# Kernel optimization log

Hardware: AMD Instinct MI355X
Metric: run time of the kernel (lower is better)

The kernel has to match this reference:

```python
import jax, jax.numpy as jnp
import numpy as np

D_MODEL = 1024
NUM_HEADS = 16
D_K = D_MODEL // NUM_HEADS


def setup_inputs() -> dict:
    key = jax.random.key(0)
    ks = jax.random.split(key, 11)
    B, S = 2, 2048
    scale = 1.0 / np.sqrt(D_MODEL)
    return {
        "Q": jax.random.normal(ks[0], (B, S, D_MODEL), jnp.float32),
        "K": jax.random.normal(ks[1], (B, S, D_MODEL), jnp.float32),
        "V": jax.random.normal(ks[2], (B, S, D_MODEL), jnp.float32),
        "Wq": jax.random.normal(ks[3], (D_MODEL, D_MODEL), jnp.float32) * scale,
        "bq": jnp.zeros((D_MODEL,), jnp.float32),
        "Wk": jax.random.normal(ks[4], (D_MODEL, D_MODEL), jnp.float32) * scale,
        "bk": jnp.zeros((D_MODEL,), jnp.float32),
        "Wv": jax.random.normal(ks[5], (D_MODEL, D_MODEL), jnp.float32) * scale,
        "bv": jnp.zeros((D_MODEL,), jnp.float32),
        "Wo": jax.random.normal(ks[6], (D_MODEL, D_MODEL), jnp.float32) * scale,
        "bo": jnp.zeros((D_MODEL,), jnp.float32),
    }


def reference(Q, K, V, Wq, bq, Wk, bk, Wv, bv, Wo, bo):
    B, S, _ = Q.shape
    # linear projections (torch Linear: x @ W.T + b)
    q = Q @ Wq.T + bq
    k = K @ Wk.T + bk
    v = V @ Wv.T + bv
    # split heads: [B, S, H, d_k] -> [B, H, S, d_k]
    q = q.reshape(B, S, NUM_HEADS, D_K).transpose(0, 2, 1, 3)
    k = k.reshape(B, S, NUM_HEADS, D_K).transpose(0, 2, 1, 3)
    v = v.reshape(B, S, NUM_HEADS, D_K).transpose(0, 2, 1, 3)
    # scaled dot-product attention, full [B, H, S, S] scores as in original
    scores = jnp.einsum("bhqd,bhkd->bhqk", q, k) / jnp.sqrt(jnp.float32(D_K))
    probs = jax.nn.softmax(scores, axis=-1)
    attn = jnp.einsum("bhqk,bhkd->bhqd", probs, v)
    # merge heads and output projection
    attn = attn.transpose(0, 2, 1, 3).reshape(B, S, D_MODEL)
    return attn @ Wo.T + bo
```

## Files before the change

### kernel.cpp

```cpp
#include <hip/hip_runtime.h>
#include <cstdint>
#include <cstddef>

#define D_MODEL 1024
#define NHEADS 16
#define DK 64
#define BATCH 2
#define SEQ 2048
#define MROWS 4096

using f32x4 = __attribute__((ext_vector_type(4))) float;
using f32x16 = __attribute__((ext_vector_type(16))) float;
using u16x8 = __attribute__((ext_vector_type(8))) unsigned short;
using u32x4 = __attribute__((ext_vector_type(4))) unsigned int;
using bf16x8 = __attribute__((ext_vector_type(8))) __bf16;

static __device__ __forceinline__ f32x4 mfma16(u16x8 a, u16x8 b, f32x4 c) {
    return __builtin_amdgcn_mfma_f32_16x16x32_bf16(
        __builtin_bit_cast(bf16x8, a), __builtin_bit_cast(bf16x8, b), c, 0, 0, 0);
}
static __device__ __forceinline__ f32x16 mfma32(u16x8 a, u16x8 b, f32x16 c) {
    return __builtin_amdgcn_mfma_f32_32x32x16_bf16(
        __builtin_bit_cast(bf16x8, a), __builtin_bit_cast(bf16x8, b), c, 0, 0, 0);
}

static __device__ __forceinline__ unsigned short f2b(float f) {
    unsigned int u = __float_as_uint(f);
    u += 0x7fffu + ((u >> 16) & 1u);
    return (unsigned short)(u >> 16);
}
static __device__ __forceinline__ unsigned int cvt_pk(float lo, float hi) {
    unsigned int r;
    asm("v_cvt_pk_bf16_f32 %0, %1, %2" : "=v"(r) : "v"(lo), "v"(hi));
    return r;
}
static __device__ __forceinline__ void plswap(unsigned int& a, unsigned int& b) {
    asm("v_permlane32_swap_b32 %0, %1" : "+v"(a), "+v"(b));
}
static __device__ __forceinline__ float fexp2(float x) {
#if __has_builtin(__builtin_amdgcn_exp2f)
    return __builtin_amdgcn_exp2f(x);
#else
    float r;
    asm("v_exp_f32 %0, %1" : "=v"(r) : "v"(x));
    return r;
#endif
}
static __device__ __forceinline__ void gll16(const void* g, void* l) {
    __builtin_amdgcn_global_load_lds(
        (const __attribute__((address_space(1))) void*)g,
        (__attribute__((address_space(3))) void*)l, 16, 0, 0);
}
#define SBAR() __builtin_amdgcn_s_barrier()
#define SCHED0() __builtin_amdgcn_sched_barrier(0)

__global__ __launch_bounds__(256) void cvtw_kernel(const float* __restrict__ w0,
                                                   const float* __restrict__ w1,
                                                   const float* __restrict__ w2,
                                                   const float* __restrict__ w3,
                                                   unsigned short* __restrict__ out,
                                                   int n4, float scale0) {
    const float* srcs[4] = {w0, w1, w2, w3};
    const float* src = srcs[blockIdx.y];
    unsigned short* dst = out + (size_t)blockIdx.y * (size_t)n4 * 4;
    float scale = (blockIdx.y == 0) ? scale0 : 1.0f;
    int i = blockIdx.x * 256 + threadIdx.x;
    if (i < n4) {
        float4 v = reinterpret_cast<const float4*>(src)[i];
        ushort4 o;
        o.x = f2b(v.x * scale);
        o.y = f2b(v.y * scale);
        o.z = f2b(v.z * scale);
        o.w = f2b(v.w * scale);
        reinterpret_cast<ushort4*>(dst)[i] = o;
    }
}


__global__ __launch_bounds__(256, 3) void gemm_qkv_kernel(
    const float* __restrict__ A0, const float* __restrict__ A1, const float* __restrict__ A2,
    const unsigned short* __restrict__ W,
    unsigned short* __restrict__ qo, unsigned short* __restrict__ ko,
    unsigned short* __restrict__ vto,
    const float* __restrict__ b0, const float* __restrict__ b1, const float* __restrict__ b2,
    float qsc) {
    __shared__ __align__(16) char Asb[8192];
    __shared__ __align__(16) char Wb[2][8192];

    const int tid = threadIdx.x;
    const int lane = tid & 63;
    const int wid = tid >> 6;
    const int wr = wid >> 1, wc = wid & 1;
    const int g = (lane >> 4) & 3, l16 = lane & 15;

    const int logical = ((int)blockIdx.x & 7) * 96 + ((int)blockIdx.x >> 3);
    const int m = logical >> 8;
    const int rem = logical & 255;
    const int y = rem >> 3, xc = rem & 7;
    const int row0 = y * 128;
    const int wrow0 = m * 1024 + xc * 128;

    const float* Af = (m == 0) ? A0 : ((m == 1) ? A1 : A2);

    const int arow = tid >> 1;
    const int ahalf = tid & 1;
    const float* asrc = Af + (size_t)(row0 + arow) * 1024 + ahalf * 16;
    const int aline = tid >> 2;
    const int apar = (tid >> 1) & 1;
    const int al7 = aline & 7;
    const int aglo = ((apar * 4 + ahalf * 2) ^ al7) * 16;
    const int aghi = ((apar * 4 + ahalf * 2 + 1) ^ al7) * 16;

    const int sline = tid >> 3;
    const int sgl = (tid & 7) ^ (sline & 7);
    const int srow = sline * 2 + (sgl >> 2);
    const int skcol = (sgl & 3) * 8;

    float4 a0r, a1r, a2r, a3r;
    auto loadA = [&](int k0) {
        const float4* s = reinterpret_cast<const float4*>(asrc + k0);
        a0r = s[0];
        a1r = s[1];
        a2r = s[2];
        a3r = s[3];
    };
    auto writeA = [&]() {
        u32x4 glo = {cvt_pk(a0r.x, a0r.y), cvt_pk(a0r.z, a0r.w),
                     cvt_pk(a1r.x, a1r.y), cvt_pk(a1r.z, a1r.w)};
        u32x4 ghi = {cvt_pk(a2r.x, a2r.y), cvt_pk(a2r.z, a2r.w),
                     cvt_pk(a3r.x, a3r.y), cvt_pk(a3r.z, a3r.w)};
        *reinterpret_cast<u32x4*>(Asb + aline * 128 + aglo) = glo;
        *reinterpret_cast<u32x4*>(Asb + aline * 128 + aghi) = ghi;
    };
    auto stageW = [&](int k0, int buf) {
        const char* w0 = (const char*)W + (size_t)(wrow0 + srow) * 2048 + (size_t)(k0 + skcol) * 2;
        gll16(w0, Wb[buf] + wid * 1024);
        gll16(w0 + (size_t)64 * 2048, Wb[buf] + 4096 + wid * 1024);
    };

    const int rswz = ((((l16 & 1) << 2) + g) ^ ((l16 >> 1) & 7)) << 4;
    const int abase = (wr * 32 + (l16 >> 1)) * 128 + rswz;
    const int bbase = (wc * 32 + (l16 >> 1)) * 128 + rswz;

    f32x4 acc[4][4] = {};

    loadA(0);
    stageW(0, 0);
    asm volatile("s_waitcnt vmcnt(2)" ::: "memory");
    SCHED0();
    writeA();
    asm volatile("s_waitcnt lgkmcnt(0)" ::: "memory");
    SCHED0();

    for (int t = 0; t < 32; ++t) {
        if (t < 31) {
            loadA((t + 1) * 32);
            stageW((t + 1) * 32, (t & 1) ^ 1);
            asm volatile("s_waitcnt vmcnt(6)" ::: "memory");
        } else {
            asm volatile("s_waitcnt vmcnt(0)" ::: "memory");
        }
        SCHED0();
        SBAR();
        SCHED0();
        u16x8 af[4], bf[4];
#pragma unroll
        for (int mi = 0; mi < 4; ++mi)
            af[mi] = *reinterpret_cast<const u16x8*>(Asb + abase + mi * 1024);
#pragma unroll
        for (int ni = 0; ni < 4; ++ni)
            bf[ni] = *reinterpret_cast<const u16x8*>(Wb[t & 1] + bbase + ni * 1024);
        __builtin_amdgcn_s_setprio(1);
#pragma unroll
        for (int mi = 0; mi < 4; ++mi)
#pragma unroll
            for (int ni = 0; ni < 4; ++ni)
                acc[mi][ni] = mfma16(af[mi], bf[ni], acc[mi][ni]);
        __builtin_amdgcn_s_setprio(0);
        if (t < 31) {
            SBAR();
            SCHED0();
            asm volatile("s_waitcnt vmcnt(2)" ::: "memory");
            SCHED0();
            writeA();
            asm volatile("s_waitcnt lgkmcnt(0)" ::: "memory");
            SCHED0();
        }
    }

    const float* bias = (m == 0) ? b0 : ((m == 1) ? b1 : b2);
    const float bsc = (m == 0) ? qsc : 1.0f;
#pragma unroll
    for (int mi = 0; mi < 4; ++mi) {
#pragma unroll
        for (int ni = 0; ni < 4; ++ni) {
            int r = row0 + wr * 64 + mi * 16 + g * 4;
            int cl = xc * 128 + wc * 64 + ni * 16 + l16;
            float bv = bsc * bias[cl];
            if (m < 2) {
                unsigned short* outp = m ? ko : qo;
#pragma unroll
                for (int j = 0; j < 4; ++j)
                    outp[(size_t)(r + j) * 1024 + cl] = f2b(acc[mi][ni][j] + bv);
            } else {
                ushort4 o;
                o.x = f2b(acc[mi][ni][0] + bv);
                o.y = f2b(acc[mi][ni][1] + bv);
                o.z = f2b(acc[mi][ni][2] + bv);
                o.w = f2b(acc[mi][ni][3] + bv);
                *reinterpret_cast<ushort4*>(vto + (size_t)cl * MROWS + r) = o;
            }
        }
    }
}

__global__ __launch_bounds__(256, 4) void gemm_out_kernel(
    const unsigned short* __restrict__ Abf,
    const unsigned short* __restrict__ W,
    float* __restrict__ fo,
    const float* __restrict__ bias) {
    __shared__ __align__(16) char Ab[2][8192];
    __shared__ __align__(16) char Wb[2][4096];

    const int tid = threadIdx.x;
    const int lane = tid & 63;
    const int wid = tid >> 6;
    const int wr = wid >> 1, wc = wid & 1;
    const int g = (lane >> 4) & 3, l16 = lane & 15;

    const int logical = ((int)blockIdx.x & 7) * 64 + ((int)blockIdx.x >> 3);
    const int y = logical >> 4, xc = logical & 15;
    const int row0 = y * 128;
    const int wrow0 = xc * 64;

    const int sline = tid >> 3;
    const int sgl = (tid & 7) ^ (sline & 7);
    const int srow = sline * 2 + (sgl >> 2);
    const int skcol = (sgl & 3) * 8;

    auto stage = [&](int k0, int buf) {
        const char* a0 = (const char*)Abf + (size_t)(row0 + srow) * 2048 + (size_t)(k0 + skcol) * 2;
        gll16(a0, Ab[buf] + wid * 1024);
        gll16(a0 + (size_t)64 * 2048, Ab[buf] + 4096 + wid * 1024);
        const char* w0 = (const char*)W + (size_t)(wrow0 + srow) * 2048 + (size_t)(k0 + skcol) * 2;
        gll16(w0, Wb[buf] + wid * 1024);
    };

    const int rswz = ((((l16 & 1) << 2) + g) ^ ((l16 >> 1) & 7)) << 4;
    const int abase = (wr * 32 + (l16 >> 1)) * 128 + rswz;
    const int bbase = (wc * 16 + (l16 >> 1)) * 128 + rswz;

    f32x4 acc[4][2] = {};
    stage(0, 0);

    for (int t = 0; t < 32; ++t) {
        if (t < 31) stage((t + 1) * 32, (t & 1) ^ 1);
        if (t < 31) asm volatile("s_waitcnt vmcnt(3)" ::: "memory");
        else asm volatile("s_waitcnt vmcnt(0)" ::: "memory");
        SCHED0();
        SBAR();
        SCHED0();
        u16x8 af[4], bf[2];
#pragma unroll
        for (int mi = 0; mi < 4; ++mi)
            af[mi] = *reinterpret_cast<const u16x8*>(Ab[t & 1] + abase + mi * 1024);
#pragma unroll
        for (int ni = 0; ni < 2; ++ni)
            bf[ni] = *reinterpret_cast<const u16x8*>(Wb[t & 1] + bbase + ni * 1024);
        __builtin_amdgcn_s_setprio(1);
#pragma unroll
        for (int mi = 0; mi < 4; ++mi)
#pragma unroll
            for (int ni = 0; ni < 2; ++ni)
                acc[mi][ni] = mfma16(af[mi], bf[ni], acc[mi][ni]);
        __builtin_amdgcn_s_setprio(0);
        SBAR();
        SCHED0();
    }

#pragma unroll
    for (int mi = 0; mi < 4; ++mi) {
#pragma unroll
        for (int ni = 0; ni < 2; ++ni) {
            int r = row0 + wr * 64 + mi * 16 + g * 4;
            int cl = xc * 64 + wc * 32 + ni * 16 + l16;
            float bv = bias[cl];
#pragma unroll
            for (int j = 0; j < 4; ++j)
                fo[(size_t)(r + j) * 1024 + cl] = acc[mi][ni][j] + bv;
        }
    }
}

__global__ __launch_bounds__(512, 2) void attn_kernel(
    const unsigned short* __restrict__ qp,
    const unsigned short* __restrict__ kp,
    const unsigned short* __restrict__ vT,
    unsigned short* __restrict__ ao) {
    __shared__ __align__(16) char lds[65536];

    const int tid = threadIdx.x;
    const int lane = tid & 63;
    const int wid = tid >> 6;
    const int wq = wid & 3, wk = wid >> 2;
    const int l31 = lane & 31, hi = lane >> 5;

    const int logical = ((int)blockIdx.x & 7) * 64 + ((int)blockIdx.x >> 3);
    const int qt = logical & 15;
    const int bh = logical >> 4;
    const int b = bh >> 4, h = bh & 15;
    const int ch = h * DK;
    const int q0 = b * SEQ + qt * 128;

    const int srow = wid * 8 + (lane >> 3);
    const int g16 = (lane & 7) ^ (lane >> 3);
    const char* kbase = (const char*)kp + ((size_t)(b * SEQ + srow)) * 2048 + ch * 2 + g16 * 16;
    const char* vbase = (const char*)vT + ((size_t)(ch + srow)) * (MROWS * 2) + (size_t)b * SEQ * 2 + g16 * 16;

    const char* qr = (const char*)qp + (size_t)(q0 + wq * 32 + l31) * 2048 + ch * 2;
    u16x8 qf[4];
#pragma unroll
    for (int t = 0; t < 4; ++t)
        qf[t] = *reinterpret_cast<const u16x8*>(qr + t * 32 + hi * 16);

    auto stageKV = [&](int kt2, char* base) {
        gll16(kbase + (size_t)kt2 * (64 * 2048), base + wid * 1024);
        gll16(kbase + (size_t)(kt2 * 64 + 1024) * 2048, base + 8192 + wid * 1024);
        gll16(vbase + kt2 * 128, base + 16384 + wid * 1024);
        gll16(vbase + kt2 * 128 + 2048, base + 24576 + wid * 1024);
    };

    const int swz = (lane & 7) << 4;
    f32x16 acco[2] = {};
    float l0 = 0.f, l1 = 0.f, l2 = 0.f, l3 = 0.f;

    stageKV(0, lds);
    for (int kt = 0; kt < 16; ++kt) {
        if (kt < 15) stageKV(kt + 1, lds + (((kt + 1) & 1) << 15));
        if (kt < 15) asm volatile("s_waitcnt vmcnt(4)" ::: "memory");
        else asm volatile("s_waitcnt vmcnt(0)" ::: "memory");
        SCHED0();
        SBAR();
        SCHED0();
        const char* cb = lds + ((kt & 1) << 15);
        const char* Kb = cb + wk * 8192;
        const char* Vb = cb + 16384 + wk * 8192;

        unsigned int pf[4][4];
#pragma unroll
        for (int ts = 0; ts < 2; ++ts) {
            f32x16 s = {};
            __builtin_amdgcn_s_setprio(1);
#pragma unroll
            for (int t = 0; t < 4; ++t) {
                u16x8 kf = *reinterpret_cast<const u16x8*>(Kb + (ts * 32 + l31) * 128 + ((32 * t + 16 * hi) ^ swz));
                s = mfma32(kf, qf[t], s);
            }
            __builtin_amdgcn_s_setprio(0);
            float p[16];
#pragma unroll
            for (int r = 0; r < 16; r += 4) {
                p[r] = fexp2(s[r]);
                p[r + 1] = fexp2(s[r + 1]);
                p[r + 2] = fexp2(s[r + 2]);
                p[r + 3] = fexp2(s[r + 3]);
                l0 += p[r];
                l1 += p[r + 1];
                l2 += p[r + 2];
                l3 += p[r + 3];
            }
#pragma unroll
            for (int i = 0; i < 2; ++i) {
                unsigned int a = cvt_pk(p[2 * i], p[2 * i + 1]);
                unsigned int bb = cvt_pk(p[4 + 2 * i], p[5 + 2 * i]);
                plswap(a, bb);
                pf[2 * ts][i] = a;
                pf[2 * ts][i + 2] = bb;
                unsigned int a2 = cvt_pk(p[8 + 2 * i], p[9 + 2 * i]);
                unsigned int b2 = cvt_pk(p[12 + 2 * i], p[13 + 2 * i]);
                plswap(a2, b2);
                pf[2 * ts + 1][i] = a2;
                pf[2 * ts + 1][i + 2] = b2;
            }
        }
        __builtin_amdgcn_s_setprio(1);
#pragma unroll
        for (int t = 0; t < 4; ++t) {
            u32x4 wv = {pf[t][0], pf[t][1], pf[t][2], pf[t][3]};
            u16x8 pfr = __builtin_bit_cast(u16x8, wv);
#pragma unroll
            for (int dt = 0; dt < 2; ++dt) {
                u16x8 vf = *reinterpret_cast<const u16x8*>(Vb + (dt * 32 + l31) * 128 + ((32 * t + 16 * hi) ^ swz));
                acco[dt] = mfma32(vf, pfr, acco[dt]);
            }
        }
        __builtin_amdgcn_s_setprio(0);
        SBAR();
        SCHED0();
    }

    float L = (l0 + l1) + (l2 + l3);

    float Lh = L + __shfl_xor(L, 32);
    float* cmb = reinterpret_cast<float*>(lds);
    float* slot = cmb + (size_t)tid * 18;
    f32x16 outg = acco[1 ^ wk];
#pragma unroll
    for (int mm = 0; mm < 8; ++mm)
        *reinterpret_cast<float2*>(slot + 2 * mm) = float2{outg[2 * mm], outg[2 * mm + 1]};
    slot[16] = Lh;
    __syncthreads();
    const float* ps = cmb + (size_t)(tid ^ 256) * 18;
    f32x16 kept = acco[wk];
#pragma unroll
    for (int mm = 0; mm < 8; ++mm) {
        float2 t2 = *reinterpret_cast<const float2*>(ps + 2 * mm);
        kept[2 * mm] += t2.x;
        kept[2 * mm + 1] += t2.y;
    }
    float rl = 1.0f / (Lh + ps[16]);
    __syncthreads();

    char* ot = lds + wid * 2304;
    const int r7 = l31 & 7;
#pragma unroll
    for (int mm = 0; mm < 4; ++mm) {
        uint2 pko;
        pko.x = cvt_pk(kept[4 * mm] * rl, kept[4 * mm + 1] * rl);
        pko.y = cvt_pk(kept[4 * mm + 2] * rl, kept[4 * mm + 3] * rl);
        *reinterpret_cast<uint2*>(ot + l31 * 72 + (((2 * mm + hi) ^ r7) << 3)) = pko;
    }
    const int rr = lane >> 1, half = lane & 1;
    const int rb7 = rr & 7;
    uint2 t0 = *reinterpret_cast<const uint2*>(ot + rr * 72 + (((half * 4 + 0) ^ rb7) << 3));
    uint2 t1 = *reinterpret_cast<const uint2*>(ot + rr * 72 + (((half * 4 + 1) ^ rb7) << 3));
    uint2 t2 = *reinterpret_cast<const uint2*>(ot + rr * 72 + (((half * 4 + 2) ^ rb7) << 3));
    uint2 t3 = *reinterpret_cast<const uint2*>(ot + rr * 72 + (((half * 4 + 3) ^ rb7) << 3));
    unsigned short* dst = ao + (size_t)(q0 + wq * 32 + rr) * 1024 + ch + wk * 32 + half * 16;
    uint4 o0 = {t0.x, t0.y, t1.x, t1.y};
    uint4 o1 = {t2.x, t2.y, t3.x, t3.y};
    *reinterpret_cast<uint4*>(dst) = o0;
    *reinterpret_cast<uint4*>(dst + 8) = o1;
}

extern "C" void kernel_launch(void* const* d_in, const int* in_sizes, int n_in,
                              void* d_out, int out_size, void* d_ws, size_t ws_size,
                              hipStream_t stream) {
    const float* Q = (const float*)d_in[0];
    const float* K = (const float*)d_in[1];
    const float* V = (const float*)d_in[2];
    const float* Wq = (const float*)d_in[3];
    const float* bq = (const float*)d_in[4];
    const float* Wk = (const float*)d_in[5];
    const float* bk = (const float*)d_in[6];
    const float* Wv = (const float*)d_in[7];
    const float* bv = (const float*)d_in[8];
    const float* Wo = (const float*)d_in[9];
    const float* bo = (const float*)d_in[10];

    unsigned short* ws = (unsigned short*)d_ws;
    const size_t SZ = (size_t)MROWS * D_MODEL;
    const size_t WSZ = (size_t)D_MODEL * D_MODEL;
    unsigned short* bufW = ws;
    unsigned short* qp = bufW + 4 * WSZ;
    unsigned short* kp = qp + SZ;
    unsigned short* vT = kp + SZ;
    unsigned short* ao = vT + SZ;

    const float qscale = 0.125f * 1.44269504088896f;

    dim3 blk(256);
    dim3 gcw((unsigned)(WSZ / 4 / 256), 4);
    cvtw_kernel<<<gcw, blk, 0, stream>>>(Wq, Wk, Wv, Wo, bufW, (int)(WSZ / 4), qscale);

    gemm_qkv_kernel<<<dim3(768), blk, 0, stream>>>(Q, K, V, bufW, qp, kp, vT, bq, bk, bv, qscale);

    attn_kernel<<<dim3(512), dim3(512), 0, stream>>>(qp, kp, vT, ao);

    gemm_out_kernel<<<dim3(512), blk, 0, stream>>>(ao, bufW + 3 * WSZ, (float*)d_out, bo);
}
```

Baseline: 129.2 us.

## Deepen QKV GEMM A-prefetch and halve attention KV tile size

The QKV projection GEMM now prefetches two k-steps ahead, ping-ponging between two register sets for the fp32 A tile and issuing W stages earlier, to hide global load latency. The attention kernel shrinks its K/V tile from 64 to 32 keys per wave-half. This cuts LDS from 64KB to 36KB, which may allow more resident blocks per CU. In exchange it doubles the loop iterations and barriers and raises register pressure in the GEMM.

```diff
diff --git a/kernel.cpp b/kernel.cpp
--- a/kernel.cpp
+++ b/kernel.cpp
@@ -53,6 +53,8 @@
 }
 #define SBAR() __builtin_amdgcn_s_barrier()
 #define SCHED0() __builtin_amdgcn_sched_barrier(0)
+#define WAITV(n) asm volatile("s_waitcnt vmcnt(" #n ")" ::: "memory")
+#define WAITL0() asm volatile("s_waitcnt lgkmcnt(0)" ::: "memory")
 
 __global__ __launch_bounds__(256) void cvtw_kernel(const float* __restrict__ w0,
                                                    const float* __restrict__ w1,
@@ -77,6 +79,8 @@
 }
 
 
+struct AReg { float4 r0, r1, r2, r3; };
+
 __global__ __launch_bounds__(256, 3) void gemm_qkv_kernel(
     const float* __restrict__ A0, const float* __restrict__ A1, const float* __restrict__ A2,
     const unsigned short* __restrict__ W,
@@ -116,19 +120,19 @@
     const int srow = sline * 2 + (sgl >> 2);
     const int skcol = (sgl & 3) * 8;
 
-    float4 a0r, a1r, a2r, a3r;
-    auto loadA = [&](int k0) {
+    AReg rA, rB;
+    auto loadTo = [&](AReg& R, int k0) {
         const float4* s = reinterpret_cast<const float4*>(asrc + k0);
-        a0r = s[0];
-        a1r = s[1];
-        a2r = s[2];
-        a3r = s[3];
-    };
-    auto writeA = [&]() {
-        u32x4 glo = {cvt_pk(a0r.x, a0r.y), cvt_pk(a0r.z, a0r.w),
-                     cvt_pk(a1r.x, a1r.y), cvt_pk(a1r.z, a1r.w)};
-        u32x4 ghi = {cvt_pk(a2r.x, a2r.y), cvt_pk(a2r.z, a2r.w),
-                     cvt_pk(a3r.x, a3r.y), cvt_pk(a3r.z, a3r.w)};
+        R.r0 = s[0];
+        R.r1 = s[1];
+        R.r2 = s[2];
+        R.r3 = s[3];
+    };
+    auto writeFrom = [&](AReg& R) {
+        u32x4 glo = {cvt_pk(R.r0.x, R.r0.y), cvt_pk(R.r0.z, R.r0.w),
+                     cvt_pk(R.r1.x, R.r1.y), cvt_pk(R.r1.z, R.r1.w)};
+        u32x4 ghi = {cvt_pk(R.r2.x, R.r2.y), cvt_pk(R.r2.z, R.r2.w),
+                     cvt_pk(R.r3.x, R.r3.y), cvt_pk(R.r3.z, R.r3.w)};
         *reinterpret_cast<u32x4*>(Asb + aline * 128 + aglo) = glo;
         *reinterpret_cast<u32x4*>(Asb + aline * 128 + aghi) = ghi;
     };
@@ -144,22 +148,22 @@
 
     f32x4 acc[4][4] = {};
 
-    loadA(0);
+    loadTo(rA, 0);
+    loadTo(rB, 32);
     stageW(0, 0);
-    asm volatile("s_waitcnt vmcnt(2)" ::: "memory");
+    stageW(32, 1);
+    WAITV(8);
     SCHED0();
-    writeA();
-    asm volatile("s_waitcnt lgkmcnt(0)" ::: "memory");
+    writeFrom(rA);
+    WAITL0();
     SCHED0();
 
-    for (int t = 0; t < 32; ++t) {
-        if (t < 31) {
-            loadA((t + 1) * 32);
-            stageW((t + 1) * 32, (t & 1) ^ 1);
-            asm volatile("s_waitcnt vmcnt(6)" ::: "memory");
-        } else {
-            asm volatile("s_waitcnt vmcnt(0)" ::: "memory");
-        }
+    auto iter = [&](int t, AReg& ld, AReg& wr_) {
+        if (t < 30) loadTo(ld, (t + 2) * 32);
+        if (t == 0) WAITV(6);
+        else if (t < 30) WAITV(10);
+        else if (t == 30) WAITV(6);
+        else WAITV(0);
         SCHED0();
         SBAR();
         SCHED0();
@@ -180,12 +184,19 @@
         if (t < 31) {
             SBAR();
             SCHED0();
-            asm volatile("s_waitcnt vmcnt(2)" ::: "memory");
+            if (t < 30) stageW((t + 2) * 32, t & 1);
+            if (t < 30) WAITV(8);
+            else WAITV(2);
             SCHED0();
-            writeA();
-            asm volatile("s_waitcnt lgkmcnt(0)" ::: "memory");
+            writeFrom(wr_);
+            WAITL0();
             SCHED0();
         }
+    };
+#pragma unroll 1
+    for (int tt = 0; tt < 16; ++tt) {
+        iter(2 * tt, rA, rB);
+        iter(2 * tt + 1, rB, rA);
     }
 
     const float* bias = (m == 0) ? b0 : ((m == 1) ? b1 : b2);
@@ -255,8 +266,8 @@
 
     for (int t = 0; t < 32; ++t) {
         if (t < 31) stage((t + 1) * 32, (t & 1) ^ 1);
-        if (t < 31) asm volatile("s_waitcnt vmcnt(3)" ::: "memory");
-        else asm volatile("s_waitcnt vmcnt(0)" ::: "memory");
+        if (t < 31) WAITV(3);
+        else WAITV(0);
         SCHED0();
         SBAR();
         SCHED0();
@@ -297,7 +308,7 @@
     const unsigned short* __restrict__ kp,
     const unsigned short* __restrict__ vT,
     unsigned short* __restrict__ ao) {
-    __shared__ __align__(16) char lds[65536];
+    __shared__ __align__(16) char lds[36864];
 
     const int tid = threadIdx.x;
     const int lane = tid & 63;
@@ -312,10 +323,15 @@
     const int ch = h * DK;
     const int q0 = b * SEQ + qt * 128;
 
-    const int srow = wid * 8 + (lane >> 3);
-    const int g16 = (lane & 7) ^ (lane >> 3);
-    const char* kbase = (const char*)kp + ((size_t)(b * SEQ + srow)) * 2048 + ch * 2 + g16 * 16;
-    const char* vbase = (const char*)vT + ((size_t)(ch + srow)) * (MROWS * 2) + (size_t)b * SEQ * 2 + g16 * 16;
+    const int kline = tid >> 3;
+    const int krow = kline & 31;
+    const int kgl = (tid & 7) ^ (krow & 7);
+    const char* ksrc = (const char*)kp +
+        ((size_t)(b * SEQ + (kline >> 5) * 1024 + krow)) * 2048 + ch * 2 + kgl * 16;
+    const int vd = tid >> 3;
+    const int vgl = (tid & 7) ^ (vd & 7);
+    const char* vsrc = (const char*)vT + ((size_t)(ch + vd)) * (MROWS * 2) +
+        ((size_t)(b * SEQ + (vgl >> 2) * 1024 + (vgl & 3) * 8)) * 2;
 
     const char* qr = (const char*)qp + (size_t)(q0 + wq * 32 + l31) * 2048 + ch * 2;
     u16x8 qf[4];
@@ -324,73 +340,74 @@
         qf[t] = *reinterpret_cast<const u16x8*>(qr + t * 32 + hi * 16);
 
     auto stageKV = [&](int kt2, char* base) {
-        gll16(kbase + (size_t)kt2 * (64 * 2048), base + wid * 1024);
-        gll16(kbase + (size_t)(kt2 * 64 + 1024) * 2048, base + 8192 + wid * 1024);
-        gll16(vbase + kt2 * 128, base + 16384 + wid * 1024);
-        gll16(vbase + kt2 * 128 + 2048, base + 24576 + wid * 1024);
-    };
-
-    const int swz = (lane & 7) << 4;
+        gll16(ksrc + (size_t)kt2 * 65536, base + wid * 1024);
+        gll16(vsrc + kt2 * 64, base + 8192 + wid * 1024);
+    };
+
+    const int sw7 = (l31 & 7);
     f32x16 acco[2] = {};
     float l0 = 0.f, l1 = 0.f, l2 = 0.f, l3 = 0.f;
 
     stageKV(0, lds);
-    for (int kt = 0; kt < 16; ++kt) {
-        if (kt < 15) stageKV(kt + 1, lds + (((kt + 1) & 1) << 15));
-        if (kt < 15) asm volatile("s_waitcnt vmcnt(4)" ::: "memory");
-        else asm volatile("s_waitcnt vmcnt(0)" ::: "memory");
+    for (int kt = 0; kt < 32; ++kt) {
+        if (kt < 31) {
+            stageKV(kt + 1, lds + (((kt + 1) & 1) << 14));
+            WAITV(2);
+        } else {
+            WAITV(0);
+        }
         SCHED0();
         SBAR();
         SCHED0();
-        const char* cb = lds + ((kt & 1) << 15);
-        const char* Kb = cb + wk * 8192;
-        const char* Vb = cb + 16384 + wk * 8192;
-
-        unsigned int pf[4][4];
-#pragma unroll
-        for (int ts = 0; ts < 2; ++ts) {
-            f32x16 s = {};
-            __builtin_amdgcn_s_setprio(1);
-#pragma unroll
-            for (int t = 0; t < 4; ++t) {
-                u16x8 kf = *reinterpret_cast<const u16x8*>(Kb + (ts * 32 + l31) * 128 + ((32 * t + 16 * hi) ^ swz));
-                s = mfma32(kf, qf[t], s);
-            }
-            __builtin_amdgcn_s_setprio(0);
-            float p[16];
-#pragma unroll
-            for (int r = 0; r < 16; r += 4) {
-                p[r] = fexp2(s[r]);
-                p[r + 1] = fexp2(s[r + 1]);
-                p[r + 2] = fexp2(s[r + 2]);
-                p[r + 3] = fexp2(s[r + 3]);
-                l0 += p[r];
-                l1 += p[r + 1];
-                l2 += p[r + 2];
-                l3 += p[r + 3];
-            }
-#pragma unroll
-            for (int i = 0; i < 2; ++i) {
-                unsigned int a = cvt_pk(p[2 * i], p[2 * i + 1]);
-                unsigned int bb = cvt_pk(p[4 + 2 * i], p[5 + 2 * i]);
-                plswap(a, bb);
-                pf[2 * ts][i] = a;
-                pf[2 * ts][i + 2] = bb;
-                unsigned int a2 = cvt_pk(p[8 + 2 * i], p[9 + 2 * i]);
-                unsigned int b2 = cvt_pk(p[12 + 2 * i], p[13 + 2 * i]);
-                plswap(a2, b2);
-                pf[2 * ts + 1][i] = a2;
-                pf[2 * ts + 1][i + 2] = b2;
-            }
-        }
+        const char* cb = lds + ((kt & 1) << 14);
+
+        f32x16 s = {};
         __builtin_amdgcn_s_setprio(1);
 #pragma unroll
         for (int t = 0; t < 4; ++t) {
-            u32x4 wv = {pf[t][0], pf[t][1], pf[t][2], pf[t][3]};
+            u16x8 kf = *reinterpret_cast<const u16x8*>(
+                cb + wk * 4096 + l31 * 128 + (((2 * t + hi) ^ sw7) << 4));
+            s = mfma32(kf, qf[t], s);
+        }
+        __builtin_amdgcn_s_setprio(0);
+
+        float p[16];
+#pragma unroll
+        for (int r = 0; r < 16; r += 4) {
+            p[r] = fexp2(s[r]);
+            p[r + 1] = fexp2(s[r + 1]);
+            p[r + 2] = fexp2(s[r + 2]);
+            p[r + 3] = fexp2(s[r + 3]);
+            l0 += p[r];
+            l1 += p[r + 1];
+            l2 += p[r + 2];
+            l3 += p[r + 3];
+        }
+        unsigned int pf0[4], pf1[4];
+#pragma unroll
+        for (int i = 0; i < 2; ++i) {
+            unsigned int a = cvt_pk(p[2 * i], p[2 * i + 1]);
+            unsigned int bb = cvt_pk(p[4 + 2 * i], p[5 + 2 * i]);
+            plswap(a, bb);
+            pf0[i] = a;
+            pf0[i + 2] = bb;
+            unsigned int a2 = cvt_pk(p[8 + 2 * i], p[9 + 2 * i]);
+            unsigned int b2 = cvt_pk(p[12 + 2 * i], p[13 + 2 * i]);
+            plswap(a2, b2);
+            pf1[i] = a2;
+            pf1[i + 2] = b2;
+        }
+
+        __builtin_amdgcn_s_setprio(1);
+#pragma unroll
+        for (int t = 0; t < 2; ++t) {
+            u32x4 wv = t ? u32x4{pf1[0], pf1[1], pf1[2], pf1[3]}
+                         : u32x4{pf0[0], pf0[1], pf0[2], pf0[3]};
             u16x8 pfr = __builtin_bit_cast(u16x8, wv);
 #pragma unroll
             for (int dt = 0; dt < 2; ++dt) {
-                u16x8 vf = *reinterpret_cast<const u16x8*>(Vb + (dt * 32 + l31) * 128 + ((32 * t + 16 * hi) ^ swz));
+                u16x8 vf = *reinterpret_cast<const u16x8*>(
+                    cb + 8192 + (dt * 32 + l31) * 128 + (((wk * 4 + 2 * t + hi) ^ sw7) << 4));
                 acco[dt] = mfma32(vf, pfr, acco[dt]);
             }
         }
```

Measured after the change: 127.5 us. About the same (-1.4%).
